# Kernel optimization log

Hardware: AMD Instinct MI355X
Metric: run time of the kernel (lower is better)

The kernel has to match this reference:

```python
import jax, jax.numpy as jnp
import numpy as np

BIT_SHIFT = 4
PROJECT = True
DIMS = [4096, 4096, 4096, 4096]
BATCH = 8192


def ternarize(w):
    # Ternary weight quantization {-1,0,+1} with straight-through estimator.
    q = jnp.clip(jnp.round(w), -1.0, 1.0)
    return w + jax.lax.stop_gradient(q - w)


def binarize(x):
    # Binary projection sign(x) with hardtanh straight-through estimator.
    c = jnp.clip(x, -1.0, 1.0)
    return c + jax.lax.stop_gradient(jnp.sign(x) - c)


def tern_bin_layer(x, w):
    # Ternary-weight matmul followed by bit-shift scaling (divide by 2**BIT_SHIFT),
    # then optional binary projection of the activation.
    scale = 1.0 / (1 << BIT_SHIFT)
    y = jnp.matmul(x, ternarize(w)) * scale
    if PROJECT:
        y = binarize(y)
    return y


def setup_inputs() -> dict:
    key = jax.random.key(0)
    ks = jax.random.split(key, 4)
    x = jax.random.normal(ks[0], (BATCH, DIMS[0]), dtype=jnp.float32)
    # Latent float weights; ternarized inside the layer.
    W0 = jax.random.normal(ks[1], (DIMS[0], DIMS[1]), dtype=jnp.float32) * 0.7
    W1 = jax.random.normal(ks[2], (DIMS[1], DIMS[2]), dtype=jnp.float32) * 0.7
    W2 = jax.random.normal(ks[3], (DIMS[2], DIMS[3]), dtype=jnp.float32) * 0.7
    return {"x": x, "W0": W0, "W1": W1, "W2": W2}


def reference(x, W0, W1, W2):
    h = tern_bin_layer(x, W0)
    h = tern_bin_layer(h, W1)
    h = tern_bin_layer(h, W2)
    return h
```

## Files before the change

kernel.cpp:

```cpp
#include <hip/hip_runtime.h>
#include <stdint.h>

#define MDIM 8192
#define KDIM 4096
#define NDIM 4096
#define MAXFLAGS (2 * 1024 * 1024)

typedef int i32x4 __attribute__((ext_vector_type(4)));

__device__ __forceinline__ void gl2lds16(const void* g, void* l) {
  __builtin_amdgcn_global_load_lds(
      (const __attribute__((address_space(1))) void*)(uintptr_t)(g),
      (__attribute__((address_space(3))) void*)(uintptr_t)(l), 16, 0, 0);
}

__global__ __launch_bounds__(256) void k_tern(const float* __restrict__ W,
                                              int8_t* __restrict__ Qt) {
  __shared__ int8_t t[64][65];
  const int n0 = blockIdx.x * 64;
  const int k0 = blockIdx.y * 64;
  const int tid = threadIdx.x;
  const int c = tid & 63;
  const int r0 = tid >> 6;
#pragma unroll
  for (int i = 0; i < 16; ++i) {
    int r = (i << 2) + r0;
    float w = W[(size_t)(k0 + r) * NDIM + (n0 + c)];
    float q = fminf(1.f, fmaxf(-1.f, rintf(w)));
    t[r][c] = (int8_t)(int)q;
  }
  __syncthreads();
#pragma unroll
  for (int i = 0; i < 16; ++i) {
    int r = (i << 2) + r0;
    Qt[(size_t)(n0 + r) * KDIM + (k0 + c)] = t[c][r];
  }
}

__global__ __launch_bounds__(256) void k_quant(const float* __restrict__ x,
                                               int8_t* __restrict__ dig) {
  const size_t P = (size_t)MDIM * KDIM;
  size_t i = ((size_t)blockIdx.x * 256 + threadIdx.x) * 4;
  float4 v = *(const float4*)(x + i);
  float f[4] = {v.x, v.y, v.z, v.w};
  int8_t dd[3][4];
#pragma unroll
  for (int j = 0; j < 4; ++j) {
    long long s = __double2ll_rn((double)f[j] * 524288.0);
    int8_t d0 = (int8_t)s; s = (s - d0) >> 8;
    int8_t d1 = (int8_t)s; s = (s - d1) >> 8;
    int8_t d2 = (int8_t)s;
    dd[0][j] = d0; dd[1][j] = d1; dd[2][j] = d2;
  }
#pragma unroll
  for (int p = 0; p < 3; ++p) {
    char4 c4; c4.x = dd[p][0]; c4.y = dd[p][1]; c4.z = dd[p][2]; c4.w = dd[p][3];
    *(char4*)(dig + p * P + i) = c4;
  }
}

__global__ void k_zero(int* c) {
  if (threadIdx.x == 0 && blockIdx.x == 0) *c = 0;
}

__global__ __launch_bounds__(512) void k_gemm_l1(const int8_t* __restrict__ dig,
                                                 const int8_t* __restrict__ Qt,
                                                 int8_t* __restrict__ h,
                                                 int* __restrict__ cnt,
                                                 int2* __restrict__ flags) {
  __shared__ __align__(16) int8_t As[2][3][64][128];
  __shared__ __align__(16) int8_t Bs[2][128][128];
  const int tid = threadIdx.x;
  const int w = tid >> 6, l = tid & 63;
  const size_t P = (size_t)MDIM * KDIM;

  const int nwg = gridDim.x;
  const int wg = (blockIdx.x & 7) * (nwg >> 3) + (blockIdx.x >> 3);
  const int NB = NDIM / 128;
  const int mb = wg / NB, nb = wg % NB;

  const int srow = tid >> 3;
  const int sswz = (tid & 7) ^ (srow & 7);
  const int8_t* a_src = dig + (size_t)(mb * 64 + srow) * KDIM + sswz * 16;
  const int8_t* b_src0 = Qt + (size_t)(nb * 128 + srow) * KDIM + sswz * 16;
  const int8_t* b_src1 = b_src0 + (size_t)64 * KDIM;

  i32x4 acc[3][2][2];
#pragma unroll
  for (int p = 0; p < 3; ++p)
#pragma unroll
    for (int mi = 0; mi < 2; ++mi)
#pragma unroll
      for (int ni = 0; ni < 2; ++ni) acc[p][mi][ni] = (i32x4){0, 0, 0, 0};

  const int wr = (w >> 2) * 32;
  const int wc = (w & 3) * 32;

  auto stage = [&](int buf, int kk) {
    int8_t* ad = &As[buf][0][0][0] + w * 1024;
    int8_t* bd = &Bs[buf][0][0] + w * 1024;
#pragma unroll
    for (int p = 0; p < 3; ++p) gl2lds16(a_src + p * P + kk, ad + p * 8192);
    gl2lds16(b_src0 + kk, bd);
    gl2lds16(b_src1 + kk, bd + 8192);
  };

  auto compute = [&](int buf) {
#pragma unroll
    for (int ki = 0; ki < 2; ++ki) {
      const int kg = ki * 4 + (l >> 4);
      i32x4 b[2];
#pragma unroll
      for (int ni = 0; ni < 2; ++ni) {
        int nr = wc + ni * 16 + (l & 15);
        b[ni] = *(const i32x4*)&Bs[buf][nr][(kg ^ (nr & 7)) * 16];
      }
      __builtin_amdgcn_s_setprio(1);
#pragma unroll
      for (int p = 0; p < 3; ++p)
#pragma unroll
        for (int mi = 0; mi < 2; ++mi) {
          int ar = wr + mi * 16 + (l & 15);
          i32x4 a = *(const i32x4*)&As[buf][p][ar][(kg ^ (ar & 7)) * 16];
#pragma unroll
          for (int ni = 0; ni < 2; ++ni)
            acc[p][mi][ni] =
                __builtin_amdgcn_mfma_i32_16x16x64_i8(a, b[ni], acc[p][mi][ni], 0, 0, 0);
        }
      __builtin_amdgcn_s_setprio(0);
    }
  };

  stage(0, 0);
  stage(1, 128);
  asm volatile("s_waitcnt vmcnt(5)" ::: "memory");
  __builtin_amdgcn_sched_barrier(0);
  __builtin_amdgcn_s_barrier();

  const int NT = KDIM / 128;
  for (int t = 0; t < NT; ++t) {
    compute(t & 1);
    if (t == NT - 1) break;
    asm volatile("s_waitcnt lgkmcnt(0)" ::: "memory");
    __builtin_amdgcn_sched_barrier(0);
    __builtin_amdgcn_s_barrier();
    if (t + 2 < NT) {
      stage(t & 1, (t + 2) * 128);
      asm volatile("s_waitcnt vmcnt(5)" ::: "memory");
    } else {
      asm volatile("s_waitcnt vmcnt(0)" ::: "memory");
    }
    __builtin_amdgcn_sched_barrier(0);
    __builtin_amdgcn_s_barrier();
  }

  const int mbase = mb * 64 + wr + ((l >> 4) << 2);
  const int nbase = nb * 128 + wc + (l & 15);
#pragma unroll
  for (int mi = 0; mi < 2; ++mi)
#pragma unroll
    for (int ni = 0; ni < 2; ++ni)
#pragma unroll
      for (int j = 0; j < 4; ++j) {
        int s0 = acc[0][mi][ni][j], s1 = acc[1][mi][ni][j];
        int s2 = acc[2][mi][ni][j];
        double d = ((double)s2 * 256.0 + (double)s1) * 256.0 + (double)s0;
        int sg = (d > 0.0) - (d < 0.0);
        int row = mbase + mi * 16 + j;
        int col = nbase + ni * 16;
        h[(size_t)row * NDIM + col] = (int8_t)sg;
        if (fabs(d) <= 2048.0) {
          int idx = atomicAdd(cnt, 1);
          if (idx < MAXFLAGS) flags[idx] = make_int2(row, col);
        }
      }
}

__global__ __launch_bounds__(256) void k_fixup(const float* __restrict__ x,
                                               const int8_t* __restrict__ Qt,
                                               const int* __restrict__ cnt,
                                               const int2* __restrict__ flags,
                                               int8_t* __restrict__ h) {
  __shared__ double red[256];
  int n = *cnt;
  if (n > MAXFLAGS) n = MAXFLAGS;
  for (int i = blockIdx.x; i < n; i += gridDim.x) {
    int2 rc = flags[i];
    const float* xr = x + (size_t)rc.x * KDIM;
    const int8_t* qr = Qt + (size_t)rc.y * KDIM;
    double s = 0.0;
    for (int k = threadIdx.x; k < KDIM; k += 256)
      s += (double)xr[k] * (double)qr[k];
    red[threadIdx.x] = s;
    __syncthreads();
#pragma unroll
    for (int st = 128; st > 0; st >>= 1) {
      if (threadIdx.x < st) red[threadIdx.x] += red[threadIdx.x + st];
      __syncthreads();
    }
    if (threadIdx.x == 0) {
      double d = red[0];
      h[(size_t)rc.x * NDIM + rc.y] = (int8_t)((d > 0.0) - (d < 0.0));
    }
    __syncthreads();
  }
}

template <int F32OUT>
__global__ __launch_bounds__(512) void k_gemm_bin(const int8_t* __restrict__ A,
                                                  const int8_t* __restrict__ Qt,
                                                  void* __restrict__ outp) {
  __shared__ __align__(16) int8_t As[2][128][128];
  __shared__ __align__(16) int8_t Bs[2][128][128];
  const int tid = threadIdx.x;
  const int w = tid >> 6, l = tid & 63;

  const int nwg = gridDim.x;
  const int wg = (blockIdx.x & 7) * (nwg >> 3) + (blockIdx.x >> 3);
  const int NB = NDIM / 128;
  const int mb = wg / NB, nb = wg % NB;

  const int srow = tid >> 3;
  const int sswz = (tid & 7) ^ (srow & 7);
  const int8_t* a0 = A + (size_t)(mb * 128 + srow) * KDIM + sswz * 16;
  const int8_t* a1 = a0 + (size_t)64 * KDIM;
  const int8_t* b0 = Qt + (size_t)(nb * 128 + srow) * KDIM + sswz * 16;
  const int8_t* b1 = b0 + (size_t)64 * KDIM;

  i32x4 acc[4][2];
#pragma unroll
  for (int mi = 0; mi < 4; ++mi)
#pragma unroll
    for (int ni = 0; ni < 2; ++ni) acc[mi][ni] = (i32x4){0, 0, 0, 0};

  const int wr = (w >> 2) * 64, wc = (w & 3) * 32;

  auto stage = [&](int buf, int kk) {
    int8_t* ad = &As[buf][0][0] + w * 1024;
    int8_t* bd = &Bs[buf][0][0] + w * 1024;
    gl2lds16(a0 + kk, ad);
    gl2lds16(a1 + kk, ad + 8192);
    gl2lds16(b0 + kk, bd);
    gl2lds16(b1 + kk, bd + 8192);
  };

  auto compute = [&](int buf) {
#pragma unroll
    for (int ki = 0; ki < 2; ++ki) {
      const int kg = ki * 4 + (l >> 4);
      i32x4 b[2];
#pragma unroll
      for (int ni = 0; ni < 2; ++ni) {
        int nr = wc + ni * 16 + (l & 15);
        b[ni] = *(const i32x4*)&Bs[buf][nr][(kg ^ (nr & 7)) * 16];
      }
      __builtin_amdgcn_s_setprio(1);
#pragma unroll
      for (int mi = 0; mi < 4; ++mi) {
        int ar = wr + mi * 16 + (l & 15);
        i32x4 a = *(const i32x4*)&As[buf][ar][(kg ^ (ar & 7)) * 16];
#pragma unroll
        for (int ni = 0; ni < 2; ++ni)
          acc[mi][ni] = __builtin_amdgcn_mfma_i32_16x16x64_i8(a, b[ni], acc[mi][ni], 0, 0, 0);
      }
      __builtin_amdgcn_s_setprio(0);
    }
  };

  stage(0, 0);
  stage(1, 128);
  asm volatile("s_waitcnt vmcnt(4)" ::: "memory");
  __builtin_amdgcn_sched_barrier(0);
  __builtin_amdgcn_s_barrier();

  const int NT = KDIM / 128;
  for (int t = 0; t < NT; ++t) {
    compute(t & 1);
    if (t == NT - 1) break;
    asm volatile("s_waitcnt lgkmcnt(0)" ::: "memory");
    __builtin_amdgcn_sched_barrier(0);
    __builtin_amdgcn_s_barrier();
    if (t + 2 < NT) {
      stage(t & 1, (t + 2) * 128);
      asm volatile("s_waitcnt vmcnt(4)" ::: "memory");
    } else {
      asm volatile("s_waitcnt vmcnt(0)" ::: "memory");
    }
    __builtin_amdgcn_sched_barrier(0);
    __builtin_amdgcn_s_barrier();
  }

  const int mbase = mb * 128 + wr + ((l >> 4) << 2);
  const int nbase = nb * 128 + wc + (l & 15);
#pragma unroll
  for (int mi = 0; mi < 4; ++mi)
#pragma unroll
    for (int ni = 0; ni < 2; ++ni)
#pragma unroll
      for (int j = 0; j < 4; ++j) {
        int s = acc[mi][ni][j];
        int sg = (s > 0) - (s < 0);
        size_t off = (size_t)(mbase + mi * 16 + j) * NDIM + (nbase + ni * 16);
        if (F32OUT)
          ((float*)outp)[off] = (float)sg;
        else
          ((int8_t*)outp)[off] = (int8_t)sg;
      }
}

extern "C" void kernel_launch(void* const* d_in, const int* in_sizes, int n_in,
                              void* d_out, int out_size, void* d_ws, size_t ws_size,
                              hipStream_t stream) {
  (void)in_sizes; (void)n_in; (void)out_size; (void)ws_size;
  const float* x  = (const float*)d_in[0];
  const float* W0 = (const float*)d_in[1];
  const float* W1 = (const float*)d_in[2];
  const float* W2 = (const float*)d_in[3];
  float* out = (float*)d_out;

  const size_t QB = (size_t)KDIM * NDIM;
  const size_t HB = (size_t)MDIM * NDIM;
  int8_t* Qt0 = (int8_t*)d_ws;
  int8_t* Qt1 = Qt0 + QB;
  int8_t* Qt2 = Qt1 + QB;
  int8_t* h0  = Qt2 + QB;
  int8_t* h1  = h0 + HB;

  int8_t* dig = (int8_t*)d_out;
  int2* flags = (int2*)((char*)d_out + 3 * HB);
  int* cnt = (int*)((char*)d_out + 3 * HB + (size_t)MAXFLAGS * 8);

  dim3 tgrid(NDIM / 64, KDIM / 64);
  k_tern<<<tgrid, 256, 0, stream>>>(W0, Qt0);
  k_tern<<<tgrid, 256, 0, stream>>>(W1, Qt1);
  k_tern<<<tgrid, 256, 0, stream>>>(W2, Qt2);
  k_quant<<<((size_t)MDIM * KDIM) / 1024, 256, 0, stream>>>(x, dig);
  k_zero<<<1, 64, 0, stream>>>(cnt);
  k_gemm_l1<<<(MDIM / 64) * (NDIM / 128), 512, 0, stream>>>(dig, Qt0, h0, cnt, flags);
  k_fixup<<<512, 256, 0, stream>>>(x, Qt0, cnt, flags, h0);
  k_gemm_bin<0><<<(MDIM / 128) * (NDIM / 128), 512, 0, stream>>>(h0, Qt1, h1);
  k_gemm_bin<1><<<(MDIM / 128) * (NDIM / 128), 512, 0, stream>>>(h1, Qt2, out);
}
```

Baseline: 803.6 us.

## Deepen GEMM pipelines to four stages with 64-wide K tiles

Both int8 MFMA GEMM kernels switch from double-buffered 128-wide K tiles to quad-buffered 64-wide K tiles, keeping three tiles of loads in flight. The LDS swizzle and the global-to-LDS staging layout are reworked to match. In the L1 kernel, warps are specialized so six warps load A digit planes and two warps load B. A launch-bounds occupancy hint of 4 is added. The aim is to hide global-load latency better, at the cost of twice as many barriers per K and possible imbalance between the A and B loading warps.

```diff
diff --git a/kernel.cpp b/kernel.cpp
--- a/kernel.cpp
+++ b/kernel.cpp
@@ -7,6 +7,10 @@
 #define MAXFLAGS (2 * 1024 * 1024)
 
 typedef int i32x4 __attribute__((ext_vector_type(4)));
+
+#define VMCNT(n) asm volatile("s_waitcnt vmcnt(" #n ")" ::: "memory")
+#define LGKMCNT0 asm volatile("s_waitcnt lgkmcnt(0)" ::: "memory")
+#define SB0 __builtin_amdgcn_sched_barrier(0)
 
 __device__ __forceinline__ void gl2lds16(const void* g, void* l) {
   __builtin_amdgcn_global_load_lds(
@@ -63,13 +67,13 @@
   if (threadIdx.x == 0 && blockIdx.x == 0) *c = 0;
 }
 
-__global__ __launch_bounds__(512) void k_gemm_l1(const int8_t* __restrict__ dig,
-                                                 const int8_t* __restrict__ Qt,
-                                                 int8_t* __restrict__ h,
-                                                 int* __restrict__ cnt,
-                                                 int2* __restrict__ flags) {
-  __shared__ __align__(16) int8_t As[2][3][64][128];
-  __shared__ __align__(16) int8_t Bs[2][128][128];
+__global__ __launch_bounds__(512, 4) void k_gemm_l1(const int8_t* __restrict__ dig,
+                                                    const int8_t* __restrict__ Qt,
+                                                    int8_t* __restrict__ h,
+                                                    int* __restrict__ cnt,
+                                                    int2* __restrict__ flags) {
+  __shared__ __align__(16) int8_t As[4][3][64][64];
+  __shared__ __align__(16) int8_t Bs[4][128][64];
   const int tid = threadIdx.x;
   const int w = tid >> 6, l = tid & 63;
   const size_t P = (size_t)MDIM * KDIM;
@@ -79,11 +83,23 @@
   const int NB = NDIM / 128;
   const int mb = wg / NB, nb = wg % NB;
 
-  const int srow = tid >> 3;
-  const int sswz = (tid & 7) ^ (srow & 7);
-  const int8_t* a_src = dig + (size_t)(mb * 64 + srow) * KDIM + sswz * 16;
-  const int8_t* b_src0 = Qt + (size_t)(nb * 128 + srow) * KDIM + sswz * 16;
-  const int8_t* b_src1 = b_src0 + (size_t)64 * KDIM;
+  const int srow_in = l >> 2;
+  const int scol = (((l & 3) ^ ((l >> 3) & 3)) << 4);
+  const bool wA = (w < 6);
+  const int8_t* ga0 = nullptr; const int8_t* ga1 = nullptr;
+  const int8_t* gb0 = nullptr; const int8_t* gb1 = nullptr;
+  const int8_t* gb2 = nullptr; const int8_t* gb3 = nullptr;
+  if (wA) {
+    int i0 = w * 2, i1 = w * 2 + 1;
+    ga0 = dig + (size_t)(i0 >> 2) * P + (size_t)(mb * 64 + (i0 & 3) * 16 + srow_in) * KDIM + scol;
+    ga1 = dig + (size_t)(i1 >> 2) * P + (size_t)(mb * 64 + (i1 & 3) * 16 + srow_in) * KDIM + scol;
+  } else {
+    int j = (w - 6) * 4;
+    gb0 = Qt + (size_t)(nb * 128 + (j + 0) * 16 + srow_in) * KDIM + scol;
+    gb1 = Qt + (size_t)(nb * 128 + (j + 1) * 16 + srow_in) * KDIM + scol;
+    gb2 = Qt + (size_t)(nb * 128 + (j + 2) * 16 + srow_in) * KDIM + scol;
+    gb3 = Qt + (size_t)(nb * 128 + (j + 3) * 16 + srow_in) * KDIM + scol;
+  }
 
   i32x4 acc[3][2][2];
 #pragma unroll
@@ -95,62 +111,67 @@
 
   const int wr = (w >> 2) * 32;
   const int wc = (w & 3) * 32;
+  const int kg = l >> 4;
+  const int fsw = ((kg ^ ((l >> 1) & 3)) << 4);
 
   auto stage = [&](int buf, int kk) {
-    int8_t* ad = &As[buf][0][0][0] + w * 1024;
-    int8_t* bd = &Bs[buf][0][0] + w * 1024;
-#pragma unroll
-    for (int p = 0; p < 3; ++p) gl2lds16(a_src + p * P + kk, ad + p * 8192);
-    gl2lds16(b_src0 + kk, bd);
-    gl2lds16(b_src1 + kk, bd + 8192);
+    if (wA) {
+      int8_t* d0 = &As[buf][0][0][0] + (w * 2) * 1024;
+      gl2lds16(ga0 + kk, d0);
+      gl2lds16(ga1 + kk, d0 + 1024);
+    } else {
+      int8_t* d0 = &Bs[buf][0][0] + ((w - 6) * 4) * 1024;
+      gl2lds16(gb0 + kk, d0);
+      gl2lds16(gb1 + kk, d0 + 1024);
+      gl2lds16(gb2 + kk, d0 + 2048);
+      gl2lds16(gb3 + kk, d0 + 3072);
+    }
   };
 
   auto compute = [&](int buf) {
-#pragma unroll
-    for (int ki = 0; ki < 2; ++ki) {
-      const int kg = ki * 4 + (l >> 4);
-      i32x4 b[2];
-#pragma unroll
-      for (int ni = 0; ni < 2; ++ni) {
-        int nr = wc + ni * 16 + (l & 15);
-        b[ni] = *(const i32x4*)&Bs[buf][nr][(kg ^ (nr & 7)) * 16];
+    i32x4 b[2];
+#pragma unroll
+    for (int ni = 0; ni < 2; ++ni) {
+      int nr = wc + ni * 16 + (l & 15);
+      b[ni] = *(const i32x4*)&Bs[buf][nr][fsw];
+    }
+    __builtin_amdgcn_s_setprio(1);
+#pragma unroll
+    for (int p = 0; p < 3; ++p)
+#pragma unroll
+      for (int mi = 0; mi < 2; ++mi) {
+        int ar = wr + mi * 16 + (l & 15);
+        i32x4 a = *(const i32x4*)&As[buf][p][ar][fsw];
+#pragma unroll
+        for (int ni = 0; ni < 2; ++ni)
+          acc[p][mi][ni] =
+              __builtin_amdgcn_mfma_i32_16x16x64_i8(a, b[ni], acc[p][mi][ni], 0, 0, 0);
       }
-      __builtin_amdgcn_s_setprio(1);
-#pragma unroll
-      for (int p = 0; p < 3; ++p)
-#pragma unroll
-        for (int mi = 0; mi < 2; ++mi) {
-          int ar = wr + mi * 16 + (l & 15);
-          i32x4 a = *(const i32x4*)&As[buf][p][ar][(kg ^ (ar & 7)) * 16];
-#pragma unroll
-          for (int ni = 0; ni < 2; ++ni)
-            acc[p][mi][ni] =
-                __builtin_amdgcn_mfma_i32_16x16x64_i8(a, b[ni], acc[p][mi][ni], 0, 0, 0);
-        }
-      __builtin_amdgcn_s_setprio(0);
-    }
+    __builtin_amdgcn_s_setprio(0);
   };
 
-  stage(0, 0);
-  stage(1, 128);
-  asm volatile("s_waitcnt vmcnt(5)" ::: "memory");
-  __builtin_amdgcn_sched_barrier(0);
+  const int NT = KDIM / 64;
+  stage(0, 0); stage(1, 64); stage(2, 128); stage(3, 192);
+  if (wA) VMCNT(6); else VMCNT(12);
+  SB0;
   __builtin_amdgcn_s_barrier();
 
-  const int NT = KDIM / 128;
   for (int t = 0; t < NT; ++t) {
-    compute(t & 1);
+    compute(t & 3);
     if (t == NT - 1) break;
-    asm volatile("s_waitcnt lgkmcnt(0)" ::: "memory");
-    __builtin_amdgcn_sched_barrier(0);
+    LGKMCNT0; SB0;
     __builtin_amdgcn_s_barrier();
-    if (t + 2 < NT) {
-      stage(t & 1, (t + 2) * 128);
-      asm volatile("s_waitcnt vmcnt(5)" ::: "memory");
+    if (t + 4 < NT) {
+      stage(t & 3, (t + 4) * 64);
+      if (wA) VMCNT(6); else VMCNT(12);
+    } else if (t + 3 < NT) {
+      if (wA) VMCNT(4); else VMCNT(8);
+    } else if (t + 2 < NT) {
+      if (wA) VMCNT(2); else VMCNT(4);
     } else {
-      asm volatile("s_waitcnt vmcnt(0)" ::: "memory");
-    }
-    __builtin_amdgcn_sched_barrier(0);
+      VMCNT(0);
+    }
+    SB0;
     __builtin_amdgcn_s_barrier();
   }
 
@@ -207,11 +228,11 @@
 }
 
 template <int F32OUT>
-__global__ __launch_bounds__(512) void k_gemm_bin(const int8_t* __restrict__ A,
-                                                  const int8_t* __restrict__ Qt,
-                                                  void* __restrict__ outp) {
-  __shared__ __align__(16) int8_t As[2][128][128];
-  __shared__ __align__(16) int8_t Bs[2][128][128];
+__global__ __launch_bounds__(512, 4) void k_gemm_bin(const int8_t* __restrict__ A,
+                                                     const int8_t* __restrict__ Qt,
+                                                     void* __restrict__ outp) {
+  __shared__ __align__(16) int8_t As[4][128][64];
+  __shared__ __align__(16) int8_t Bs[4][128][64];
   const int tid = threadIdx.x;
   const int w = tid >> 6, l = tid & 63;
 
@@ -220,12 +241,10 @@
   const int NB = NDIM / 128;
   const int mb = wg / NB, nb = wg % NB;
 
-  const int srow = tid >> 3;
-  const int sswz = (tid & 7) ^ (srow & 7);
-  const int8_t* a0 = A + (size_t)(mb * 128 + srow) * KDIM + sswz * 16;
-  const int8_t* a1 = a0 + (size_t)64 * KDIM;
-  const int8_t* b0 = Qt + (size_t)(nb * 128 + srow) * KDIM + sswz * 16;
-  const int8_t* b1 = b0 + (size_t)64 * KDIM;
+  const int srow_in = l >> 2;
+  const int scol = (((l & 3) ^ ((l >> 3) & 3)) << 4);
+  const int8_t* ga = A + (size_t)(mb * 128 + w * 16 + srow_in) * KDIM + scol;
+  const int8_t* gb = Qt + (size_t)(nb * 128 + w * 16 + srow_in) * KDIM + scol;
 
   i32x4 acc[4][2];
 #pragma unroll
@@ -234,59 +253,55 @@
     for (int ni = 0; ni < 2; ++ni) acc[mi][ni] = (i32x4){0, 0, 0, 0};
 
   const int wr = (w >> 2) * 64, wc = (w & 3) * 32;
+  const int kg = l >> 4;
+  const int fsw = ((kg ^ ((l >> 1) & 3)) << 4);
 
   auto stage = [&](int buf, int kk) {
-    int8_t* ad = &As[buf][0][0] + w * 1024;
-    int8_t* bd = &Bs[buf][0][0] + w * 1024;
-    gl2lds16(a0 + kk, ad);
-    gl2lds16(a1 + kk, ad + 8192);
-    gl2lds16(b0 + kk, bd);
-    gl2lds16(b1 + kk, bd + 8192);
+    gl2lds16(ga + kk, &As[buf][0][0] + w * 1024);
+    gl2lds16(gb + kk, &Bs[buf][0][0] + w * 1024);
   };
 
   auto compute = [&](int buf) {
-#pragma unroll
-    for (int ki = 0; ki < 2; ++ki) {
-      const int kg = ki * 4 + (l >> 4);
-      i32x4 b[2];
-#pragma unroll
-      for (int ni = 0; ni < 2; ++ni) {
-        int nr = wc + ni * 16 + (l & 15);
-        b[ni] = *(const i32x4*)&Bs[buf][nr][(kg ^ (nr & 7)) * 16];
-      }
-      __builtin_amdgcn_s_setprio(1);
-#pragma unroll
-      for (int mi = 0; mi < 4; ++mi) {
-        int ar = wr + mi * 16 + (l & 15);
-        i32x4 a = *(const i32x4*)&As[buf][ar][(kg ^ (ar & 7)) * 16];
-#pragma unroll
-        for (int ni = 0; ni < 2; ++ni)
-          acc[mi][ni] = __builtin_amdgcn_mfma_i32_16x16x64_i8(a, b[ni], acc[mi][ni], 0, 0, 0);
-      }
-      __builtin_amdgcn_s_setprio(0);
-    }
+    i32x4 b[2];
+#pragma unroll
+    for (int ni = 0; ni < 2; ++ni) {
+      int nr = wc + ni * 16 + (l & 15);
+      b[ni] = *(const i32x4*)&Bs[buf][nr][fsw];
+    }
+    __builtin_amdgcn_s_setprio(1);
+#pragma unroll
+    for (int mi = 0; mi < 4; ++mi) {
+      int ar = wr + mi * 16 + (l & 15);
+      i32x4 a = *(const i32x4*)&As[buf][ar][fsw];
+#pragma unroll
+      for (int ni = 0; ni < 2; ++ni)
+        acc[mi][ni] = __builtin_amdgcn_mfma_i32_16x16x64_i8(a, b[ni], acc[mi][ni], 0, 0, 0);
+    }
+    __builtin_amdgcn_s_setprio(0);
   };
 
-  stage(0, 0);
-  stage(1, 128);
-  asm volatile("s_waitcnt vmcnt(4)" ::: "memory");
-  __builtin_amdgcn_sched_barrier(0);
+  const int NT = KDIM / 64;
+  stage(0, 0); stage(1, 64); stage(2, 128); stage(3, 192);
+  VMCNT(6);
+  SB0;
   __builtin_amdgcn_s_barrier();
 
-  const int NT = KDIM / 128;
   for (int t = 0; t < NT; ++t) {
-    compute(t & 1);
+    compute(t & 3);
     if (t == NT - 1) break;
-    asm volatile("s_waitcnt lgkmcnt(0)" ::: "memory");
-    __builtin_amdgcn_sched_barrier(0);
+    LGKMCNT0; SB0;
     __builtin_amdgcn_s_barrier();
-    if (t + 2 < NT) {
-      stage(t & 1, (t + 2) * 128);
-      asm volatile("s_waitcnt vmcnt(4)" ::: "memory");
+    if (t + 4 < NT) {
+      stage(t & 3, (t + 4) * 64);
+      VMCNT(6);
+    } else if (t + 3 < NT) {
+      VMCNT(4);
+    } else if (t + 2 < NT) {
+      VMCNT(2);
     } else {
-      asm volatile("s_waitcnt vmcnt(0)" ::: "memory");
-    }
-    __builtin_amdgcn_sched_barrier(0);
+      VMCNT(0);
+    }
+    SB0;
     __builtin_amdgcn_s_barrier();
   }
 
```

After: 928.7 us. +15.6%, slower.

## Enlarge int8 GEMM tiles and split digit planes across waves in layer one

Applied to the files above, without the earlier changes.

The binary GEMM moves to 256x256 block tiles, with each wave computing a 128x64 sub-tile and double-buffering 128KB of LDS. This raises operand reuse and cuts global and LDS traffic per MFMA. The first-layer GEMM now uses 12 waves with a 64x256 tile, where each group of four waves owns one digit plane. The planes are combined through an LDS reduction before the sign and flagging epilogue. The cost is fewer blocks per CU (one, given the LDS size), higher register pressure, and extra barriers in the epilogue.

```diff
diff --git a/kernel.cpp b/kernel.cpp
--- a/kernel.cpp
+++ b/kernel.cpp
@@ -7,6 +7,10 @@
 #define MAXFLAGS (2 * 1024 * 1024)
 
 typedef int i32x4 __attribute__((ext_vector_type(4)));
+
+#define VMCNT(n) asm volatile("s_waitcnt vmcnt(" #n ")" ::: "memory")
+#define LGKMCNT0 asm volatile("s_waitcnt lgkmcnt(0)" ::: "memory")
+#define SB0 __builtin_amdgcn_sched_barrier(0)
 
 __device__ __forceinline__ void gl2lds16(const void* g, void* l) {
   __builtin_amdgcn_global_load_lds(
@@ -63,117 +67,153 @@
   if (threadIdx.x == 0 && blockIdx.x == 0) *c = 0;
 }
 
-__global__ __launch_bounds__(512) void k_gemm_l1(const int8_t* __restrict__ dig,
-                                                 const int8_t* __restrict__ Qt,
-                                                 int8_t* __restrict__ h,
-                                                 int* __restrict__ cnt,
-                                                 int2* __restrict__ flags) {
-  __shared__ __align__(16) int8_t As[2][3][64][128];
-  __shared__ __align__(16) int8_t Bs[2][128][128];
+__global__ __launch_bounds__(768, 3) void k_gemm_l1(const int8_t* __restrict__ dig,
+                                                    const int8_t* __restrict__ Qt,
+                                                    int8_t* __restrict__ h,
+                                                    int* __restrict__ cnt,
+                                                    int2* __restrict__ flags) {
+  __shared__ __align__(16) int8_t smem[114688];
   const int tid = threadIdx.x;
   const int w = tid >> 6, l = tid & 63;
   const size_t P = (size_t)MDIM * KDIM;
 
   const int nwg = gridDim.x;
   const int wg = (blockIdx.x & 7) * (nwg >> 3) + (blockIdx.x >> 3);
-  const int NB = NDIM / 128;
+  const int NB = NDIM / 256;
   const int mb = wg / NB, nb = wg % NB;
-
-  const int srow = tid >> 3;
-  const int sswz = (tid & 7) ^ (srow & 7);
-  const int8_t* a_src = dig + (size_t)(mb * 64 + srow) * KDIM + sswz * 16;
-  const int8_t* b_src0 = Qt + (size_t)(nb * 128 + srow) * KDIM + sswz * 16;
-  const int8_t* b_src1 = b_src0 + (size_t)64 * KDIM;
-
-  i32x4 acc[3][2][2];
-#pragma unroll
-  for (int p = 0; p < 3; ++p)
-#pragma unroll
-    for (int mi = 0; mi < 2; ++mi)
-#pragma unroll
-      for (int ni = 0; ni < 2; ++ni) acc[p][mi][ni] = (i32x4){0, 0, 0, 0};
-
-  const int wr = (w >> 2) * 32;
-  const int wc = (w & 3) * 32;
+  const int p = w >> 2, q = w & 3;
+  const int wc = q * 64;
+
+  const int cs = ((l & 7) ^ ((l >> 3) & 7)) << 4;
+  const int8_t* gsrc[5];
+  int doff[5];
+#pragma unroll
+  for (int s = 0; s < 5; ++s) {
+    int i = w + 12 * s;
+    if (i >= 56) { gsrc[s] = nullptr; doff[s] = 0; continue; }
+    int r = i * 8 + (l >> 3);
+    const int8_t* base;
+    if (i < 24) base = dig + (size_t)(r >> 6) * P + (size_t)(mb * 64 + (r & 63)) * KDIM;
+    else        base = Qt + (size_t)(nb * 256 + (r - 192)) * KDIM;
+    gsrc[s] = base + cs;
+    doff[s] = i * 1024 + l * 16;
+  }
+
+  i32x4 acc[4][4];
+#pragma unroll
+  for (int mi = 0; mi < 4; ++mi)
+#pragma unroll
+    for (int ni = 0; ni < 4; ++ni) acc[mi][ni] = (i32x4){0, 0, 0, 0};
 
   auto stage = [&](int buf, int kk) {
-    int8_t* ad = &As[buf][0][0][0] + w * 1024;
-    int8_t* bd = &Bs[buf][0][0] + w * 1024;
-#pragma unroll
-    for (int p = 0; p < 3; ++p) gl2lds16(a_src + p * P + kk, ad + p * 8192);
-    gl2lds16(b_src0 + kk, bd);
-    gl2lds16(b_src1 + kk, bd + 8192);
+#pragma unroll
+    for (int s = 0; s < 5; ++s) {
+      int i = w + 12 * s;
+      if (i < 56) gl2lds16(gsrc[s] + kk, smem + buf * 57344 + doff[s]);
+    }
   };
 
   auto compute = [&](int buf) {
+    const int8_t* sb = smem + buf * 57344;
 #pragma unroll
     for (int ki = 0; ki < 2; ++ki) {
       const int kg = ki * 4 + (l >> 4);
-      i32x4 b[2];
-#pragma unroll
-      for (int ni = 0; ni < 2; ++ni) {
+      i32x4 b[4], a[4];
+#pragma unroll
+      for (int ni = 0; ni < 4; ++ni) {
         int nr = wc + ni * 16 + (l & 15);
-        b[ni] = *(const i32x4*)&Bs[buf][nr][(kg ^ (nr & 7)) * 16];
+        b[ni] = *(const i32x4*)(sb + 24576 + nr * 128 + ((kg ^ (nr & 7)) << 4));
+      }
+#pragma unroll
+      for (int mi = 0; mi < 4; ++mi) {
+        int ar = mi * 16 + (l & 15);
+        a[mi] = *(const i32x4*)(sb + p * 8192 + ar * 128 + ((kg ^ (ar & 7)) << 4));
       }
       __builtin_amdgcn_s_setprio(1);
 #pragma unroll
-      for (int p = 0; p < 3; ++p)
-#pragma unroll
-        for (int mi = 0; mi < 2; ++mi) {
-          int ar = wr + mi * 16 + (l & 15);
-          i32x4 a = *(const i32x4*)&As[buf][p][ar][(kg ^ (ar & 7)) * 16];
-#pragma unroll
-          for (int ni = 0; ni < 2; ++ni)
-            acc[p][mi][ni] =
-                __builtin_amdgcn_mfma_i32_16x16x64_i8(a, b[ni], acc[p][mi][ni], 0, 0, 0);
-        }
+      for (int mi = 0; mi < 4; ++mi)
+#pragma unroll
+        for (int ni = 0; ni < 4; ++ni)
+          acc[mi][ni] =
+              __builtin_amdgcn_mfma_i32_16x16x64_i8(a[mi], b[ni], acc[mi][ni], 0, 0, 0);
       __builtin_amdgcn_s_setprio(0);
     }
   };
 
-  stage(0, 0);
-  stage(1, 128);
-  asm volatile("s_waitcnt vmcnt(5)" ::: "memory");
-  __builtin_amdgcn_sched_barrier(0);
-  __builtin_amdgcn_s_barrier();
-
   const int NT = KDIM / 128;
+  stage(0, 0); stage(1, 128);
+  if (w < 8) VMCNT(5); else VMCNT(4);
+  SB0;
+  __builtin_amdgcn_s_barrier();
+
   for (int t = 0; t < NT; ++t) {
     compute(t & 1);
     if (t == NT - 1) break;
-    asm volatile("s_waitcnt lgkmcnt(0)" ::: "memory");
-    __builtin_amdgcn_sched_barrier(0);
+    LGKMCNT0; SB0;
     __builtin_amdgcn_s_barrier();
     if (t + 2 < NT) {
       stage(t & 1, (t + 2) * 128);
-      asm volatile("s_waitcnt vmcnt(5)" ::: "memory");
+      if (w < 8) VMCNT(5); else VMCNT(4);
     } else {
-      asm volatile("s_waitcnt vmcnt(0)" ::: "memory");
-    }
-    __builtin_amdgcn_sched_barrier(0);
+      VMCNT(0);
+    }
+    SB0;
     __builtin_amdgcn_s_barrier();
   }
 
-  const int mbase = mb * 64 + wr + ((l >> 4) << 2);
-  const int nbase = nb * 128 + wc + (l & 15);
-#pragma unroll
-  for (int mi = 0; mi < 2; ++mi)
-#pragma unroll
-    for (int ni = 0; ni < 2; ++ni)
-#pragma unroll
-      for (int j = 0; j < 4; ++j) {
-        int s0 = acc[0][mi][ni][j], s1 = acc[1][mi][ni][j];
-        int s2 = acc[2][mi][ni][j];
-        double d = ((double)s2 * 256.0 + (double)s1) * 256.0 + (double)s0;
-        int sg = (d > 0.0) - (d < 0.0);
-        int row = mbase + mi * 16 + j;
-        int col = nbase + ni * 16;
-        h[(size_t)row * NDIM + col] = (int8_t)sg;
-        if (fabs(d) <= 2048.0) {
-          int idx = atomicAdd(cnt, 1);
-          if (idx < MAXFLAGS) flags[idx] = make_int2(row, col);
+  LGKMCNT0; SB0;
+  __builtin_amdgcn_s_barrier();
+  if (p == 1) {
+#pragma unroll
+    for (int mi = 0; mi < 4; ++mi)
+#pragma unroll
+      for (int ni = 0; ni < 4; ++ni)
+        *(i32x4*)(smem + q * 16384 + ((mi * 4 + ni) * 64 + l) * 16) = acc[mi][ni];
+  }
+  LGKMCNT0; SB0;
+  __builtin_amdgcn_s_barrier();
+  if (p == 0) {
+#pragma unroll
+    for (int mi = 0; mi < 4; ++mi)
+#pragma unroll
+      for (int ni = 0; ni < 4; ++ni) {
+        i32x4 s1 = *(const i32x4*)(smem + q * 16384 + ((mi * 4 + ni) * 64 + l) * 16);
+        acc[mi][ni] += (s1 << 8);
+      }
+  }
+  LGKMCNT0; SB0;
+  __builtin_amdgcn_s_barrier();
+  if (p == 2) {
+#pragma unroll
+    for (int mi = 0; mi < 4; ++mi)
+#pragma unroll
+      for (int ni = 0; ni < 4; ++ni)
+        *(i32x4*)(smem + q * 16384 + ((mi * 4 + ni) * 64 + l) * 16) = acc[mi][ni];
+  }
+  LGKMCNT0; SB0;
+  __builtin_amdgcn_s_barrier();
+  if (p == 0) {
+    const int mbase = mb * 64 + ((l >> 4) << 2);
+    const int nbase = nb * 256 + q * 64 + (l & 15);
+#pragma unroll
+    for (int mi = 0; mi < 4; ++mi)
+#pragma unroll
+      for (int ni = 0; ni < 4; ++ni) {
+        i32x4 s2 = *(const i32x4*)(smem + q * 16384 + ((mi * 4 + ni) * 64 + l) * 16);
+#pragma unroll
+        for (int j = 0; j < 4; ++j) {
+          double dd = (double)s2[j] * 65536.0 + (double)acc[mi][ni][j];
+          int sg = (dd > 0.0) - (dd < 0.0);
+          int row = mbase + mi * 16 + j;
+          int col = nbase + ni * 16;
+          h[(size_t)row * NDIM + col] = (int8_t)sg;
+          if (fabs(dd) <= 2048.0) {
+            int idx = atomicAdd(cnt, 1);
+            if (idx < MAXFLAGS) flags[idx] = make_int2(row, col);
+          }
         }
       }
+  }
 }
 
 __global__ __launch_bounds__(256) void k_fixup(const float* __restrict__ x,
@@ -207,95 +247,99 @@
 }
 
 template <int F32OUT>
-__global__ __launch_bounds__(512) void k_gemm_bin(const int8_t* __restrict__ A,
-                                                  const int8_t* __restrict__ Qt,
-                                                  void* __restrict__ outp) {
-  __shared__ __align__(16) int8_t As[2][128][128];
-  __shared__ __align__(16) int8_t Bs[2][128][128];
+__global__ __launch_bounds__(512, 2) void k_gemm_bin(const int8_t* __restrict__ A,
+                                                     const int8_t* __restrict__ Qt,
+                                                     void* __restrict__ outp) {
+  __shared__ __align__(16) int8_t smem[131072];
   const int tid = threadIdx.x;
   const int w = tid >> 6, l = tid & 63;
 
   const int nwg = gridDim.x;
   const int wg = (blockIdx.x & 7) * (nwg >> 3) + (blockIdx.x >> 3);
-  const int NB = NDIM / 128;
+  const int NB = NDIM / 256;
   const int mb = wg / NB, nb = wg % NB;
 
-  const int srow = tid >> 3;
-  const int sswz = (tid & 7) ^ (srow & 7);
-  const int8_t* a0 = A + (size_t)(mb * 128 + srow) * KDIM + sswz * 16;
-  const int8_t* a1 = a0 + (size_t)64 * KDIM;
-  const int8_t* b0 = Qt + (size_t)(nb * 128 + srow) * KDIM + sswz * 16;
-  const int8_t* b1 = b0 + (size_t)64 * KDIM;
-
-  i32x4 acc[4][2];
-#pragma unroll
-  for (int mi = 0; mi < 4; ++mi)
-#pragma unroll
-    for (int ni = 0; ni < 2; ++ni) acc[mi][ni] = (i32x4){0, 0, 0, 0};
-
-  const int wr = (w >> 2) * 64, wc = (w & 3) * 32;
+  const int cs = ((l & 7) ^ ((l >> 3) & 7)) << 4;
+  const int r0 = w * 32 + (l >> 3);
+  const int8_t* gA[4];
+  const int8_t* gB[4];
+#pragma unroll
+  for (int s = 0; s < 4; ++s) {
+    gA[s] = A + (size_t)(mb * 256 + r0 + s * 8) * KDIM + cs;
+    gB[s] = Qt + (size_t)(nb * 256 + r0 + s * 8) * KDIM + cs;
+  }
+  const int dA = w * 4096 + l * 16;
+
+  i32x4 acc[8][4];
+#pragma unroll
+  for (int mi = 0; mi < 8; ++mi)
+#pragma unroll
+    for (int ni = 0; ni < 4; ++ni) acc[mi][ni] = (i32x4){0, 0, 0, 0};
+
+  const int wr = (w >> 2) * 128, wc = (w & 3) * 64;
 
   auto stage = [&](int buf, int kk) {
-    int8_t* ad = &As[buf][0][0] + w * 1024;
-    int8_t* bd = &Bs[buf][0][0] + w * 1024;
-    gl2lds16(a0 + kk, ad);
-    gl2lds16(a1 + kk, ad + 8192);
-    gl2lds16(b0 + kk, bd);
-    gl2lds16(b1 + kk, bd + 8192);
+    int8_t* sb = smem + buf * 65536;
+#pragma unroll
+    for (int s = 0; s < 4; ++s) gl2lds16(gA[s] + kk, sb + dA + s * 1024);
+#pragma unroll
+    for (int s = 0; s < 4; ++s) gl2lds16(gB[s] + kk, sb + 32768 + dA + s * 1024);
   };
 
   auto compute = [&](int buf) {
+    const int8_t* sb = smem + buf * 65536;
 #pragma unroll
     for (int ki = 0; ki < 2; ++ki) {
       const int kg = ki * 4 + (l >> 4);
-      i32x4 b[2];
-#pragma unroll
-      for (int ni = 0; ni < 2; ++ni) {
+      i32x4 b[4], a[8];
+#pragma unroll
+      for (int ni = 0; ni < 4; ++ni) {
         int nr = wc + ni * 16 + (l & 15);
-        b[ni] = *(const i32x4*)&Bs[buf][nr][(kg ^ (nr & 7)) * 16];
+        b[ni] = *(const i32x4*)(sb + 32768 + nr * 128 + ((kg ^ (nr & 7)) << 4));
+      }
+#pragma unroll
+      for (int mi = 0; mi < 8; ++mi) {
+        int ar = wr + mi * 16 + (l & 15);
+        a[mi] = *(const i32x4*)(sb + ar * 128 + ((kg ^ (ar & 7)) << 4));
       }
       __builtin_amdgcn_s_setprio(1);
 #pragma unroll
-      for (int mi = 0; mi < 4; ++mi) {
-        int ar = wr + mi * 16 + (l & 15);
-        i32x4 a = *(const i32x4*)&As[buf][ar][(kg ^ (ar & 7)) * 16];
-#pragma unroll
-        for (int ni = 0; ni < 2; ++ni)
-          acc[mi][ni] = __builtin_amdgcn_mfma_i32_16x16x64_i8(a, b[ni], acc[mi][ni], 0, 0, 0);
-      }
+      for (int mi = 0; mi < 8; ++mi)
+#pragma unroll
+        for (int ni = 0; ni < 4; ++ni)
+          acc[mi][ni] =
+              __builtin_amdgcn_mfma_i32_16x16x64_i8(a[mi], b[ni], acc[mi][ni], 0, 0, 0);
       __builtin_amdgcn_s_setprio(0);
     }
   };
 
-  stage(0, 0);
-  stage(1, 128);
-  asm volatile("s_waitcnt vmcnt(4)" ::: "memory");
-  __builtin_amdgcn_sched_barrier(0);
-  __builtin_amdgcn_s_barrier();
-
   const int NT = KDIM / 128;
+  stage(0, 0); stage(1, 128);
+  VMCNT(8);
+  SB0;
+  __builtin_amdgcn_s_barrier();
+
   for (int t = 0; t < NT; ++t) {
     compute(t & 1);
     if (t == NT - 1) break;
-    asm volatile("s_waitcnt lgkmcnt(0)" ::: "memory");
-    __builtin_amdgcn_sched_barrier(0);
+    LGKMCNT0; SB0;
     __builtin_amdgcn_s_barrier();
     if (t + 2 < NT) {
       stage(t & 1, (t + 2) * 128);
-      asm volatile("s_waitcnt vmcnt(4)" ::: "memory");
+      VMCNT(8);
     } else {
-      asm volatile("s_waitcnt vmcnt(0)" ::: "memory");
-    }
-    __builtin_amdgcn_sched_barrier(0);
+      VMCNT(0);
+    }
+    SB0;
     __builtin_amdgcn_s_barrier();
   }
 
-  const int mbase = mb * 128 + wr + ((l >> 4) << 2);
-  const int nbase = nb * 128 + wc + (l & 15);
-#pragma unroll
-  for (int mi = 0; mi < 4; ++mi)
-#pragma unroll
-    for (int ni = 0; ni < 2; ++ni)
+  const int mbase = mb * 256 + wr + ((l >> 4) << 2);
+  const int nbase = nb * 256 + wc + (l & 15);
+#pragma unroll
+  for (int mi = 0; mi < 8; ++mi)
+#pragma unroll
+    for (int ni = 0; ni < 4; ++ni)
 #pragma unroll
       for (int j = 0; j < 4; ++j) {
         int s = acc[mi][ni][j];
@@ -336,8 +380,8 @@
   k_tern<<<tgrid, 256, 0, stream>>>(W2, Qt2);
   k_quant<<<((size_t)MDIM * KDIM) / 1024, 256, 0, stream>>>(x, dig);
   k_zero<<<1, 64, 0, stream>>>(cnt);
-  k_gemm_l1<<<(MDIM / 64) * (NDIM / 128), 512, 0, stream>>>(dig, Qt0, h0, cnt, flags);
+  k_gemm_l1<<<(MDIM / 64) * (NDIM / 256), 768, 0, stream>>>(dig, Qt0, h0, cnt, flags);
   k_fixup<<<512, 256, 0, stream>>>(x, Qt0, cnt, flags, h0);
-  k_gemm_bin<0><<<(MDIM / 128) * (NDIM / 128), 512, 0, stream>>>(h0, Qt1, h1);
-  k_gemm_bin<1><<<(MDIM / 128) * (NDIM / 128), 512, 0, stream>>>(h1, Qt2, out);
-}
+  k_gemm_bin<0><<<(MDIM / 256) * (NDIM / 256), 512, 0, stream>>>(h0, Qt1, h1);
+  k_gemm_bin<1><<<(MDIM / 256) * (NDIM / 256), 512, 0, stream>>>(h1, Qt2, out);
+}
```

Measured after the change: 794.0 us. About the same (-1.2%).

## Enlarge binary-layer GEMM tiles to 256x256 with 8x4 MFMA per wave

Applied to the files above, without the earlier changes.

The int8 GEMM for layers two and three now uses a 256x256 output tile per workgroup instead of 128x128. Each wave holds 8x4 accumulator fragments and loads all A/B fragments before issuing the MFMAs, with a 128KB double-buffered LDS stage. This raises arithmetic intensity and cuts global traffic per output, but the grid shrinks to 512 workgroups and register and LDS pressure rise, which may limit occupancy to one block per CU.

```diff
diff --git a/kernel.cpp b/kernel.cpp
--- a/kernel.cpp
+++ b/kernel.cpp
@@ -7,6 +7,10 @@
 #define MAXFLAGS (2 * 1024 * 1024)
 
 typedef int i32x4 __attribute__((ext_vector_type(4)));
+
+#define VMCNT(n) asm volatile("s_waitcnt vmcnt(" #n ")" ::: "memory")
+#define LGKMCNT0 asm volatile("s_waitcnt lgkmcnt(0)" ::: "memory")
+#define SB0 __builtin_amdgcn_sched_barrier(0)
 
 __device__ __forceinline__ void gl2lds16(const void* g, void* l) {
   __builtin_amdgcn_global_load_lds(
@@ -133,24 +137,23 @@
 
   stage(0, 0);
   stage(1, 128);
-  asm volatile("s_waitcnt vmcnt(5)" ::: "memory");
-  __builtin_amdgcn_sched_barrier(0);
+  VMCNT(5);
+  SB0;
   __builtin_amdgcn_s_barrier();
 
   const int NT = KDIM / 128;
   for (int t = 0; t < NT; ++t) {
     compute(t & 1);
     if (t == NT - 1) break;
-    asm volatile("s_waitcnt lgkmcnt(0)" ::: "memory");
-    __builtin_amdgcn_sched_barrier(0);
+    LGKMCNT0; SB0;
     __builtin_amdgcn_s_barrier();
     if (t + 2 < NT) {
       stage(t & 1, (t + 2) * 128);
-      asm volatile("s_waitcnt vmcnt(5)" ::: "memory");
+      VMCNT(5);
     } else {
-      asm volatile("s_waitcnt vmcnt(0)" ::: "memory");
-    }
-    __builtin_amdgcn_sched_barrier(0);
+      VMCNT(0);
+    }
+    SB0;
     __builtin_amdgcn_s_barrier();
   }
 
@@ -207,95 +210,99 @@
 }
 
 template <int F32OUT>
-__global__ __launch_bounds__(512) void k_gemm_bin(const int8_t* __restrict__ A,
-                                                  const int8_t* __restrict__ Qt,
-                                                  void* __restrict__ outp) {
-  __shared__ __align__(16) int8_t As[2][128][128];
-  __shared__ __align__(16) int8_t Bs[2][128][128];
+__global__ __launch_bounds__(512, 2) void k_gemm_bin(const int8_t* __restrict__ A,
+                                                     const int8_t* __restrict__ Qt,
+                                                     void* __restrict__ outp) {
+  __shared__ __align__(16) int8_t smem[131072];
   const int tid = threadIdx.x;
   const int w = tid >> 6, l = tid & 63;
 
   const int nwg = gridDim.x;
   const int wg = (blockIdx.x & 7) * (nwg >> 3) + (blockIdx.x >> 3);
-  const int NB = NDIM / 128;
+  const int NB = NDIM / 256;
   const int mb = wg / NB, nb = wg % NB;
 
-  const int srow = tid >> 3;
-  const int sswz = (tid & 7) ^ (srow & 7);
-  const int8_t* a0 = A + (size_t)(mb * 128 + srow) * KDIM + sswz * 16;
-  const int8_t* a1 = a0 + (size_t)64 * KDIM;
-  const int8_t* b0 = Qt + (size_t)(nb * 128 + srow) * KDIM + sswz * 16;
-  const int8_t* b1 = b0 + (size_t)64 * KDIM;
-
-  i32x4 acc[4][2];
-#pragma unroll
-  for (int mi = 0; mi < 4; ++mi)
-#pragma unroll
-    for (int ni = 0; ni < 2; ++ni) acc[mi][ni] = (i32x4){0, 0, 0, 0};
-
-  const int wr = (w >> 2) * 64, wc = (w & 3) * 32;
+  const int cs = ((l & 7) ^ ((l >> 3) & 7)) << 4;
+  const int r0 = w * 32 + (l >> 3);
+  const int8_t* gA[4];
+  const int8_t* gB[4];
+#pragma unroll
+  for (int s = 0; s < 4; ++s) {
+    gA[s] = A + (size_t)(mb * 256 + r0 + s * 8) * KDIM + cs;
+    gB[s] = Qt + (size_t)(nb * 256 + r0 + s * 8) * KDIM + cs;
+  }
+  const int dA = w * 4096 + l * 16;
+
+  i32x4 acc[8][4];
+#pragma unroll
+  for (int mi = 0; mi < 8; ++mi)
+#pragma unroll
+    for (int ni = 0; ni < 4; ++ni) acc[mi][ni] = (i32x4){0, 0, 0, 0};
+
+  const int wr = (w >> 2) * 128, wc = (w & 3) * 64;
 
   auto stage = [&](int buf, int kk) {
-    int8_t* ad = &As[buf][0][0] + w * 1024;
-    int8_t* bd = &Bs[buf][0][0] + w * 1024;
-    gl2lds16(a0 + kk, ad);
-    gl2lds16(a1 + kk, ad + 8192);
-    gl2lds16(b0 + kk, bd);
-    gl2lds16(b1 + kk, bd + 8192);
+    int8_t* sb = smem + buf * 65536;
+#pragma unroll
+    for (int s = 0; s < 4; ++s) gl2lds16(gA[s] + kk, sb + dA + s * 1024);
+#pragma unroll
+    for (int s = 0; s < 4; ++s) gl2lds16(gB[s] + kk, sb + 32768 + dA + s * 1024);
   };
 
   auto compute = [&](int buf) {
+    const int8_t* sb = smem + buf * 65536;
 #pragma unroll
     for (int ki = 0; ki < 2; ++ki) {
       const int kg = ki * 4 + (l >> 4);
-      i32x4 b[2];
-#pragma unroll
-      for (int ni = 0; ni < 2; ++ni) {
+      i32x4 b[4], a[8];
+#pragma unroll
+      for (int ni = 0; ni < 4; ++ni) {
         int nr = wc + ni * 16 + (l & 15);
-        b[ni] = *(const i32x4*)&Bs[buf][nr][(kg ^ (nr & 7)) * 16];
+        b[ni] = *(const i32x4*)(sb + 32768 + nr * 128 + ((kg ^ (nr & 7)) << 4));
+      }
+#pragma unroll
+      for (int mi = 0; mi < 8; ++mi) {
+        int ar = wr + mi * 16 + (l & 15);
+        a[mi] = *(const i32x4*)(sb + ar * 128 + ((kg ^ (ar & 7)) << 4));
       }
       __builtin_amdgcn_s_setprio(1);
 #pragma unroll
-      for (int mi = 0; mi < 4; ++mi) {
-        int ar = wr + mi * 16 + (l & 15);
-        i32x4 a = *(const i32x4*)&As[buf][ar][(kg ^ (ar & 7)) * 16];
-#pragma unroll
-        for (int ni = 0; ni < 2; ++ni)
-          acc[mi][ni] = __builtin_amdgcn_mfma_i32_16x16x64_i8(a, b[ni], acc[mi][ni], 0, 0, 0);
-      }
+      for (int mi = 0; mi < 8; ++mi)
+#pragma unroll
+        for (int ni = 0; ni < 4; ++ni)
+          acc[mi][ni] =
+              __builtin_amdgcn_mfma_i32_16x16x64_i8(a[mi], b[ni], acc[mi][ni], 0, 0, 0);
       __builtin_amdgcn_s_setprio(0);
     }
   };
 
-  stage(0, 0);
-  stage(1, 128);
-  asm volatile("s_waitcnt vmcnt(4)" ::: "memory");
-  __builtin_amdgcn_sched_barrier(0);
+  const int NT = KDIM / 128;
+  stage(0, 0); stage(1, 128);
+  VMCNT(8);
+  SB0;
   __builtin_amdgcn_s_barrier();
 
-  const int NT = KDIM / 128;
   for (int t = 0; t < NT; ++t) {
     compute(t & 1);
     if (t == NT - 1) break;
-    asm volatile("s_waitcnt lgkmcnt(0)" ::: "memory");
-    __builtin_amdgcn_sched_barrier(0);
+    LGKMCNT0; SB0;
     __builtin_amdgcn_s_barrier();
     if (t + 2 < NT) {
       stage(t & 1, (t + 2) * 128);
-      asm volatile("s_waitcnt vmcnt(4)" ::: "memory");
+      VMCNT(8);
     } else {
-      asm volatile("s_waitcnt vmcnt(0)" ::: "memory");
-    }
-    __builtin_amdgcn_sched_barrier(0);
+      VMCNT(0);
+    }
+    SB0;
     __builtin_amdgcn_s_barrier();
   }
 
-  const int mbase = mb * 128 + wr + ((l >> 4) << 2);
-  const int nbase = nb * 128 + wc + (l & 15);
-#pragma unroll
-  for (int mi = 0; mi < 4; ++mi)
-#pragma unroll
-    for (int ni = 0; ni < 2; ++ni)
+  const int mbase = mb * 256 + wr + ((l >> 4) << 2);
+  const int nbase = nb * 256 + wc + (l & 15);
+#pragma unroll
+  for (int mi = 0; mi < 8; ++mi)
+#pragma unroll
+    for (int ni = 0; ni < 4; ++ni)
 #pragma unroll
       for (int j = 0; j < 4; ++j) {
         int s = acc[mi][ni][j];
@@ -338,6 +345,6 @@
   k_zero<<<1, 64, 0, stream>>>(cnt);
   k_gemm_l1<<<(MDIM / 64) * (NDIM / 128), 512, 0, stream>>>(dig, Qt0, h0, cnt, flags);
   k_fixup<<<512, 256, 0, stream>>>(x, Qt0, cnt, flags, h0);
-  k_gemm_bin<0><<<(MDIM / 128) * (NDIM / 128), 512, 0, stream>>>(h0, Qt1, h1);
-  k_gemm_bin<1><<<(MDIM / 128) * (NDIM / 128), 512, 0, stream>>>(h1, Qt2, out);
-}
+  k_gemm_bin<0><<<(MDIM / 256) * (NDIM / 256), 512, 0, stream>>>(h0, Qt1, h1);
+  k_gemm_bin<1><<<(MDIM / 256) * (NDIM / 256), 512, 0, stream>>>(h1, Qt2, out);
+}
```

Result: faster. 753.5 us (-6.2%).
